# Optimization experiments

Hardware: AMD Instinct MI355X
Metric: run time of the kernel (lower is better)

Reference implementation:

```python
import jax, jax.numpy as jnp
import numpy as np

K = 20
EPS = 1e-5

def get_graph_feature(x, k):
    # x: [B, C, N] -> edge features [B, 2C, N, k]
    xt = jnp.swapaxes(x, 1, 2)  # [B, N, C]
    sq = jnp.sum(xt * xt, axis=-1)  # [B, N]
    # negative squared distance: -(|a|^2 + |b|^2 - 2 a.b)
    pair = 2.0 * jnp.einsum('bnc,bmc->bnm', xt, xt) - sq[:, :, None] - sq[:, None, :]
    idx = jax.lax.top_k(pair, k)[1]  # [B, N, k] nearest neighbors (incl. self)
    neigh = jax.vmap(lambda f, i: f[i])(xt, idx)  # [B, N, k, C]
    ctr = xt[:, :, None, :]  # [B, N, 1, C]
    edge = jnp.concatenate([neigh - ctr, jnp.broadcast_to(ctr, neigh.shape)], axis=-1)  # [B,N,k,2C]
    return jnp.transpose(edge, (0, 3, 1, 2))  # [B, 2C, N, k]

def bn_lrelu(y, g, b, axes):
    # training-mode batchnorm (biased batch stats) + LeakyReLU(0.2)
    m = jnp.mean(y, axis=axes, keepdims=True)
    v = jnp.var(y, axis=axes, keepdims=True)
    shape = [1, -1] + [1] * (y.ndim - 2)
    yn = (y - m) / jnp.sqrt(v + EPS) * g.reshape(shape) + b.reshape(shape)
    return jnp.where(yn >= 0, yn, 0.2 * yn)

def edge_block(x, w, g, b, k):
    e = get_graph_feature(x, k)           # [B, 2C, N, k]
    y = jnp.einsum('bcnk,oc->bonk', e, w)  # 1x1 conv2d, no bias
    y = bn_lrelu(y, g, b, (0, 2, 3))
    return jnp.max(y, axis=-1)            # max over k -> [B, O, N]

def setup_inputs() -> dict:
    key = jax.random.key(0)
    ks = jax.random.split(key, 8)
    B, N = 8, 1024
    num_features = 256
    def w(k_, o, i):
        return jax.random.normal(k_, (o, i), dtype=jnp.float32) * (1.0 / np.sqrt(i))
    d = {
        'x': jax.random.normal(ks[0], (B, N, 3), dtype=jnp.float32),
        'w1': w(ks[1], 64, 6),   'g1': jnp.ones(64),  'b1': jnp.zeros(64),
        'w2': w(ks[2], 64, 128), 'g2': jnp.ones(64),  'b2': jnp.zeros(64),
        'w3': w(ks[3], 128, 128),'g3': jnp.ones(128), 'b3': jnp.zeros(128),
        'w4': w(ks[4], 256, 256),'g4': jnp.ones(256), 'b4': jnp.zeros(256),
        'w5': w(ks[5], 512, 512),'g5': jnp.ones(512), 'b5': jnp.zeros(512),
        'wemb': w(ks[6], num_features, 512),
    }
    return d

def reference(x, w1, g1, b1, w2, g2, b2, w3, g3, b3, w4, g4, b4, w5, g5, b5, wemb):
    xc = jnp.swapaxes(x, 2, 1)  # [B, 3, N]
    x1 = edge_block(xc, w1, g1, b1, K)  # [B, 64, N]
    x2 = edge_block(x1, w2, g2, b2, K)  # [B, 64, N]
    x3 = edge_block(x2, w3, g3, b3, K)  # [B, 128, N]
    x4 = edge_block(x3, w4, g4, b4, K)  # [B, 256, N]
    cat = jnp.concatenate([x1, x2, x3, x4], axis=1)  # [B, 512, N]
    y = jnp.einsum('bcn,oc->bon', cat, w5)            # 1x1 conv1d
    y = bn_lrelu(y, g5, b5, (0, 2))
    feat = jnp.max(y, axis=-1)  # [B, 512]
    return feat @ wemb.T        # [B, num_features]
```

## Files before the change

### kernel.cpp

```cpp
#include <hip/hip_runtime.h>
#include <hip/hip_bf16.h>
#include <math.h>

#define BB 8
#define NN 1024
#define KNNK 20
#define LDC 512

typedef __attribute__((ext_vector_type(8))) short bfrag8;
typedef __attribute__((ext_vector_type(4))) float facc4;
typedef __attribute__((ext_vector_type(2))) float v2f;

struct bh8 { __hip_bfloat16 h[8]; };

__device__ __forceinline__ bh8 cvt8(float4 a, float4 b) {
    bh8 v;
    v.h[0] = __float2bfloat16(a.x); v.h[1] = __float2bfloat16(a.y);
    v.h[2] = __float2bfloat16(a.z); v.h[3] = __float2bfloat16(a.w);
    v.h[4] = __float2bfloat16(b.x); v.h[5] = __float2bfloat16(b.y);
    v.h[6] = __float2bfloat16(b.z); v.h[7] = __float2bfloat16(b.w);
    return v;
}

template<int CTRL, int RMASK>
__device__ __forceinline__ float fmax_dpp(float x) {
    int xi = __float_as_int(x);
    int yi = __builtin_amdgcn_update_dpp(xi, xi, CTRL, RMASK, 0xF, false);
    return fmaxf(x, __int_as_float(yi));
}

__device__ __forceinline__ float wave_max64(float x) {
    x = fmax_dpp<0x121, 0xF>(x);
    x = fmax_dpp<0x122, 0xF>(x);
    x = fmax_dpp<0x124, 0xF>(x);
    x = fmax_dpp<0x128, 0xF>(x);
    x = fmax_dpp<0x142, 0xA>(x);
    x = fmax_dpp<0x143, 0xC>(x);
    return __int_as_float(__builtin_amdgcn_readlane(__float_as_int(x), 63));
}

__device__ __forceinline__ void select20_pf(float (*dist)[1024],
                                            int q0, int w, int lane,
                                            int* __restrict__ idxout) {
    float d[2][16];
    int   sl[2][16];
#pragma unroll
    for (int qi = 0; qi < 2; qi++) {
        int row = w * 2 + qi;
#pragma unroll
        for (int j = 0; j < 16; j++) { d[qi][j] = dist[row][lane + 64 * j]; sl[qi][j] = j; }
    }
    constexpr unsigned char CA[63] = {
        0,2,4,6,8,10,12,14,
        0,1,4,5,8,9,12,13,
        1,5,9,13,
        0,1,2,3,8,9,10,11,
        2,3,10,11,
        1,3,5,9,11,13,
        0,1,2,3,4,5,6,7,
        4,5,6,7,
        2,3,6,7,10,11,
        1,3,5,7,9,11,13};
    constexpr unsigned char CB[63] = {
        1,3,5,7,9,11,13,15,
        2,3,6,7,10,11,14,15,
        2,6,10,14,
        4,5,6,7,12,13,14,15,
        4,5,12,13,
        2,4,6,10,12,14,
        8,9,10,11,12,13,14,15,
        8,9,10,11,
        4,5,8,9,12,13,
        2,4,6,8,10,12,14};
#pragma unroll
    for (int c = 0; c < 63; c++) {
        const int a = CA[c], bq = CB[c];
#pragma unroll
        for (int qi = 0; qi < 2; qi++) {
            bool sw = d[qi][a] < d[qi][bq];
            float dmx = sw ? d[qi][bq] : d[qi][a];
            float dmn = sw ? d[qi][a]  : d[qi][bq];
            d[qi][a] = dmx; d[qi][bq] = dmn;
            int smx = sw ? sl[qi][bq] : sl[qi][a];
            int smn = sw ? sl[qi][a]  : sl[qi][bq];
            sl[qi][a] = smx; sl[qi][bq] = smn;
        }
    }
    unsigned long long slp[2];
#pragma unroll
    for (int qi = 0; qi < 2; qi++) {
        int row = w * 2 + qi;
#pragma unroll
        for (int j = 0; j < 16; j++) dist[row][j * 64 + lane] = d[qi][j];
        unsigned long long p = 0;
#pragma unroll
        for (int j = 0; j < 16; j++) p |= (unsigned long long)sl[qi][j] << (4 * j);
        slp[qi] = p;
    }
    float head[2] = {d[0][0], d[1][0]};
    float pf[2]   = {d[0][1], d[1][1]};
    int   ptr[2]  = {2, 2};
    for (int t = 0; t < KNNK; t++) {
#pragma unroll
        for (int qi = 0; qi < 2; qi++) {
            int row = w * 2 + qi;
            float bv = wave_max64(head[qi]);
            unsigned long long ball = __ballot(head[qi] == bv);
            int wl = (int)__builtin_ctzll(ball);
            bool win = (lane == wl);
            if (win) {
                idxout[(q0 + row) * KNNK + t] = (int)(slp[qi] & 15ull) * 64 + lane;
            }
            head[qi] = win ? pf[qi] : head[qi];
            slp[qi]  = win ? (slp[qi] >> 4) : slp[qi];
            if (win) {
                int p = ptr[qi];
                pf[qi] = (p < 16) ? dist[row][p * 64 + lane] : -INFINITY;
                ptr[qi] = p + 1;
            }
        }
    }
}

__device__ __forceinline__ void zero_r1(float* r1s, float* r1q, int O, int tid) {
    for (int i = tid; i < 32 * O; i += 256) { r1s[i] = 0.f; r1q[i] = 0.f; }
}

__global__ __launch_bounds__(256, 4) void knn3_fused(const float* __restrict__ x,
                                                     const float* __restrict__ w1,
                                                     float* __restrict__ zf,
                                                     int* __restrict__ idxout,
                                                     float* __restrict__ r1s, float* __restrict__ r1q) {
    __shared__ float dist[8][1024];
    int tid = threadIdx.x;
    int q0 = (blockIdx.x & 7) * 1024 + (blockIdx.x >> 3) * 8;
    int b = q0 >> 10;
    if (blockIdx.x == 0) zero_r1(r1s, r1q, 64, tid);
    const float* xb = x + (size_t)b * NN * 3;
    int lane = tid & 63, w = tid >> 6;
    float qx[8], qy[8], qz[8];
#pragma unroll
    for (int q = 0; q < 8; q++) {
        const float* qr = xb + (size_t)((q0 & (NN - 1)) + q) * 3;
        qx[q] = qr[0]; qy[q] = qr[1]; qz[q] = qr[2];
    }
#pragma unroll
    for (int cq = 0; cq < 4; cq++) {
        int cand = w * 256 + cq * 64 + lane;
        const float* cr = xb + (size_t)cand * 3;
        float cx = cr[0], cy = cr[1], cz = cr[2];
        float sqc = 0.f;
        sqc += cx * cx; sqc += cy * cy; sqc += cz * cz;
#pragma unroll
        for (int q = 0; q < 8; q++) {
            float d = qx[q] * cx + qy[q] * cy + qz[q] * cz;
            dist[q][cand] = 2.f * d - sqc;
        }
    }
    for (int i = tid; i < 8 * 128; i += 256) {
        int lq = i >> 7, j = i & 127;
        const float* wr = w1 + (j < 64 ? j * 6 : (j - 64) * 6 + 3);
        const float* xr = x + (size_t)(q0 + lq) * 3;
        zf[(size_t)(q0 + lq) * 128 + j] = wr[0] * xr[0] + wr[1] * xr[1] + wr[2] * xr[2];
    }
    __syncthreads();
    select20_pf(dist, q0, w, lane, idxout);
}

template<int C>
__device__ __forceinline__ void knn_body(const float* __restrict__ xT,
                                         const float* __restrict__ xt, int off,
                                         const float* __restrict__ sqn,
                                         int* __restrict__ idxout,
                                         float (*dist)[1024],
                                         float* qsT_raw, int knnBlk) {
    float (*qsT)[8] = (float (*)[8])qsT_raw;
    int tid = threadIdx.x;
    int q0 = (knnBlk & 7) * 1024 + (knnBlk >> 3) * 8;
    int b = q0 >> 10;
    const float* xb = xt + (size_t)b * NN * LDC + off;
    for (int j = tid; j < 2 * C; j += 256) {
        int c = j % C, ph = j / C;
        int pb = (q0 & (NN - 1)) + ph * 4;
        float4 v;
        v.x = xb[(size_t)(pb + 0) * LDC + c];
        v.y = xb[(size_t)(pb + 1) * LDC + c];
        v.z = xb[(size_t)(pb + 2) * LDC + c];
        v.w = xb[(size_t)(pb + 3) * LDC + c];
        *(float4*)&qsT[c][ph * 4] = v;
    }
    __syncthreads();
    int lane = tid & 63, w = tid >> 6;
    int cand0 = w * 256 + 4 * lane;
    const float* xTb = xT + (size_t)b * C * 1024;
    float4 sq4 = *(const float4*)(sqn + b * NN + cand0);
    v2f acc2[4][4];
#pragma unroll
    for (int j = 0; j < 4; j++)
#pragma unroll
        for (int p = 0; p < 4; p++) acc2[j][p] = (v2f){0.f, 0.f};
    for (int cg = 0; cg < C / 4; cg++) {
        float4 rch[4];
#pragma unroll
        for (int c = 0; c < 4; c++)
            rch[c] = *(const float4*)(xTb + (size_t)(4 * cg + c) * 1024 + cand0);
#pragma unroll
        for (int c = 0; c < 4; c++) {
            float4 qa = *(const float4*)&qsT[4 * cg + c][0];
            float4 qb = *(const float4*)&qsT[4 * cg + c][4];
            v2f qp[4] = {{qa.x, qa.y}, {qa.z, qa.w}, {qb.x, qb.y}, {qb.z, qb.w}};
            float rj[4] = {rch[c].x, rch[c].y, rch[c].z, rch[c].w};
#pragma unroll
            for (int j = 0; j < 4; j++) {
                v2f rr = {rj[j], rj[j]};
                acc2[j][0] += rr * qp[0];
                acc2[j][1] += rr * qp[1];
                acc2[j][2] += rr * qp[2];
                acc2[j][3] += rr * qp[3];
            }
        }
    }
#pragma unroll
    for (int p = 0; p < 4; p++)
#pragma unroll
        for (int half = 0; half < 2; half++) {
            int q = 2 * p + half;
            float4 dv;
            dv.x = 2.f * acc2[0][p][half] - sq4.x;
            dv.y = 2.f * acc2[1][p][half] - sq4.y;
            dv.z = 2.f * acc2[2][p][half] - sq4.z;
            dv.w = 2.f * acc2[3][p][half] - sq4.w;
            *(float4*)&dist[q][cand0] = dv;
        }
    __syncthreads();
    select20_pf(dist, q0, w, lane, idxout);
}

template<int C, int ZO2>
__global__ __launch_bounds__(256, 4) void knnz_fat(const float* __restrict__ xT,
                                                   const float* __restrict__ xt, int off,
                                                   const float* __restrict__ sqn,
                                                   int* __restrict__ idxout,
                                                   const float* __restrict__ w,
                                                   float* __restrict__ zf,
                                                   float* __restrict__ r1s, float* __restrict__ r1q,
                                                   int Onext) {
    __shared__ float dist[8][1024];
    __shared__ __align__(16) float qsT_raw[C * 8];
    int tid = threadIdx.x;
    if ((int)blockIdx.x < BB * NN / 8) {
        knn_body<C>(xT, xt, off, sqn, idxout, dist, qsT_raw, blockIdx.x);
        return;
    }
    constexpr int ZO = ZO2 / 2;
    int zblk = blockIdx.x - BB * NN / 8;
    if (zblk == 0) zero_r1(r1s, r1q, Onext, tid);
    float (*xs)[C] = (float (*)[C])&dist[0][0];
    int p0 = zblk * 16;
    for (int j = tid; j < 16 * (C / 4); j += 256) {
        int p = j / (C / 4), c4 = j % (C / 4);
        *(float4*)&xs[p][4 * c4] = *(const float4*)(xt + (size_t)(p0 + p) * LDC + off + 4 * c4);
    }
    __syncthreads();
    for (int j = tid; j < ZO2; j += 256) {
        const float* wr = w + (j < ZO ? (size_t)j * 2 * C : (size_t)(j - ZO) * 2 * C + C);
        float acc[16];
#pragma unroll
        for (int p = 0; p < 16; p++) acc[p] = 0.f;
        for (int c4 = 0; c4 < C / 4; c4++) {
            float4 wv = *(const float4*)(wr + 4 * c4);
#pragma unroll
            for (int p = 0; p < 16; p++) {
                float4 xv = *(const float4*)&xs[p][4 * c4];
                acc[p] += wv.x * xv.x + wv.y * xv.y + wv.z * xv.z + wv.w * xv.w;
            }
        }
#pragma unroll
        for (int p = 0; p < 16; p++) zf[(size_t)(p0 + p) * ZO2 + j] = acc[p];
    }
}

template<int C>
__global__ __launch_bounds__(256, 4) void knn_fused(const float* __restrict__ xT,
                                                    const float* __restrict__ xt, int off,
                                                    const float* __restrict__ sqn,
                                                    int* __restrict__ idxout,
                                                    float* __restrict__ r1s, float* __restrict__ r1q,
                                                    int Onext) {
    __shared__ float dist[8][1024];
    __shared__ __align__(16) float qsT_raw[C * 8];
    if (blockIdx.x == 0) zero_r1(r1s, r1q, Onext, threadIdx.x);
    knn_body<C>(xT, xt, off, sqn, idxout, dist, qsT_raw, blockIdx.x);
}

__global__ __launch_bounds__(256) void zgemm4_mfma(const float* __restrict__ xtcat,
                                                   const float* __restrict__ w4,
                                                   __hip_bfloat16* __restrict__ zf4) {
    __shared__ __hip_bfloat16 A[128][72];
    __shared__ __hip_bfloat16 W[128][72];
    int mt = blockIdx.x >> 2, nt = blockIdx.x & 3;
    int tid = threadIdx.x;
    int lane = tid & 63, wvx = tid >> 6;
    int mw = wvx >> 1, nw = wvx & 1;
    int m0 = lane & 15, qd = lane >> 4;
    int r = tid & 127, hf = tid >> 7;
    facc4 acc[4][4];
    facc4 zz = {0.f, 0.f, 0.f, 0.f};
#pragma unroll
    for (int mi = 0; mi < 4; mi++)
#pragma unroll
        for (int ni = 0; ni < 4; ni++) acc[mi][ni] = zz;
    int j = nt * 128 + r;
    const float* wsrc = w4 + (j < 256 ? (size_t)j * 256 : (size_t)(j - 256) * 256 + 128);
    const float* asrc = xtcat + (size_t)(mt * 128 + r) * 512 + 128;
    for (int kc = 0; kc < 2; kc++) {
#pragma unroll
        for (int u = 0; u < 4; u++) {
            int c0 = kc * 64 + hf * 32 + 8 * u;
            float4 a0 = *(const float4*)(asrc + c0);
            float4 a1 = *(const float4*)(asrc + c0 + 4);
            *(bh8*)&A[r][hf * 32 + 8 * u] = cvt8(a0, a1);
            float4 w0 = *(const float4*)(wsrc + c0);
            float4 w1 = *(const float4*)(wsrc + c0 + 4);
            *(bh8*)&W[r][hf * 32 + 8 * u] = cvt8(w0, w1);
        }
        __syncthreads();
#pragma unroll
        for (int kk = 0; kk < 2; kk++) {
            bfrag8 af[4], bf[4];
#pragma unroll
            for (int mi = 0; mi < 4; mi++)
                af[mi] = *(const bfrag8*)&A[64 * mw + 16 * mi + m0][32 * kk + 8 * qd];
#pragma unroll
            for (int ni = 0; ni < 4; ni++)
                bf[ni] = *(const bfrag8*)&W[64 * nw + 16 * ni + m0][32 * kk + 8 * qd];
#pragma unroll
            for (int mi = 0; mi < 4; mi++)
#pragma unroll
                for (int ni = 0; ni < 4; ni++)
                    acc[mi][ni] = __builtin_amdgcn_mfma_f32_16x16x32_bf16(af[mi], bf[ni], acc[mi][ni], 0, 0, 0);
        }
        __syncthreads();
    }
#pragma unroll
    for (int mi = 0; mi < 4; mi++)
#pragma unroll
        for (int ni = 0; ni < 4; ni++)
#pragma unroll
            for (int rg = 0; rg < 4; rg++) {
                int row = mt * 128 + mw * 64 + mi * 16 + qd * 4 + rg;
                int col = nt * 128 + nw * 64 + ni * 16 + m0;
                zf4[(size_t)row * 512 + col] = __float2bfloat16(acc[mi][ni][rg]);
            }
}

template<int O2>
__global__ __launch_bounds__(256) void gatherstats_k(const float* __restrict__ zf,
                                                     const int* __restrict__ idx,
                                                     float* __restrict__ ymax, float* __restrict__ ymin,
                                                     float* __restrict__ r1s, float* __restrict__ r1q) {
    constexpr int O = O2 / 2;
    __shared__ float red_s[4][O], red_q[4][O];
    int wv = threadIdx.x >> 6, lane = threadIdx.x & 63;
    int n = (blockIdx.x & 7) * 1024 + (blockIdx.x >> 3) * 4 + wv;
    int b = n >> 10;
    const float* zbatch = zf + (size_t)b * NN * O2;
    int nb[KNNK];
#pragma unroll
    for (int k = 0; k < KNNK; k++) nb[k] = idx[n * KNNK + k];
#pragma unroll
    for (int ch = 0; ch < O / 64; ch++) {
        int o = ch * 64 + lane;
        float g[KNNK];
#pragma unroll
        for (int k = 0; k < KNNK; k++) g[k] = zbatch[(size_t)nb[k] * O2 + o];
        float mx = -INFINITY, mn = INFINITY, s = 0.f, ss = 0.f;
#pragma unroll
        for (int k = 0; k < KNNK; k++) {
            float v = g[k];
            mx = fmaxf(mx, v); mn = fminf(mn, v); s += v; ss += v * v;
        }
        float zn  = zf[(size_t)n * O2 + o];
        float zbn = zf[(size_t)n * O2 + O + o];
        float d = zbn - zn;
        mx += d; mn += d;
        ss = ss + 2.f * d * s + (float)KNNK * d * d;
        s  = s + (float)KNNK * d;
        ymax[(size_t)n * O + o] = mx;
        ymin[(size_t)n * O + o] = mn;
        red_s[wv][o] = s;
        red_q[wv][o] = ss;
    }
    __syncthreads();
    int bucket = blockIdx.x & 31;
    for (int o = threadIdx.x; o < O; o += 256) {
        float s4 = red_s[0][o] + red_s[1][o] + red_s[2][o] + red_s[3][o];
        float q4 = red_q[0][o] + red_q[1][o] + red_q[2][o] + red_q[3][o];
        atomicAdd(&r1s[(size_t)bucket * O + o], s4);
        atomicAdd(&r1q[(size_t)bucket * O + o], q4);
    }
}

__global__ __launch_bounds__(256) void gatherstats4_k(const __hip_bfloat16* __restrict__ zf4,
                                                      const int* __restrict__ idx,
                                                      float* __restrict__ ymax, float* __restrict__ ymin,
                                                      float* __restrict__ r1s, float* __restrict__ r1q) {
    __shared__ float red_s[4][256], red_q[4][256];
    int wv = threadIdx.x >> 6, lane = threadIdx.x & 63;
    int n = (blockIdx.x & 7) * 1024 + (blockIdx.x >> 3) * 4 + wv;
    int b = n >> 10;
    const __hip_bfloat16* zbatch = zf4 + (size_t)b * NN * 512;
    int nb[KNNK];
#pragma unroll
    for (int k = 0; k < KNNK; k++) nb[k] = idx[n * KNNK + k];
#pragma unroll
    for (int ch = 0; ch < 4; ch++) {
        int o = ch * 64 + lane;
        float g[KNNK];
#pragma unroll
        for (int k = 0; k < KNNK; k++) g[k] = __bfloat162float(zbatch[(size_t)nb[k] * 512 + o]);
        float mx = -INFINITY, mn = INFINITY, s = 0.f, ss = 0.f;
#pragma unroll
        for (int k = 0; k < KNNK; k++) {
            float v = g[k];
            mx = fmaxf(mx, v); mn = fminf(mn, v); s += v; ss += v * v;
        }
        float zn  = __bfloat162float(zf4[(size_t)n * 512 + o]);
        float zbn = __bfloat162float(zf4[(size_t)n * 512 + 256 + o]);
        float d = zbn - zn;
        mx += d; mn += d;
        ss = ss + 2.f * d * s + (float)KNNK * d * d;
        s  = s + (float)KNNK * d;
        ymax[(size_t)n * 256 + o] = mx;
        ymin[(size_t)n * 256 + o] = mn;
        red_s[wv][o] = s;
        red_q[wv][o] = ss;
    }
    __syncthreads();
    int bucket = blockIdx.x & 31;
    for (int o = threadIdx.x; o < 256; o += 256) {
        float s4 = red_s[0][o] + red_s[1][o] + red_s[2][o] + red_s[3][o];
        float q4 = red_q[0][o] + red_q[1][o] + red_q[2][o] + red_q[3][o];
        atomicAdd(&r1s[(size_t)bucket * 256 + o], s4);
        atomicAdd(&r1q[(size_t)bucket * 256 + o], q4);
    }
}

template<int O>
__global__ __launch_bounds__(256) void epitrans2_k(const float* __restrict__ ymax, const float* __restrict__ ymin,
                                                   const float* __restrict__ r1s, const float* __restrict__ r1q,
                                                   const float* __restrict__ g, const float* __restrict__ beta,
                                                   double invM,
                                                   float* __restrict__ xtcat, int off_out,
                                                   float* __restrict__ xT, float* __restrict__ sqn,
                                                   __hip_bfloat16* __restrict__ xbf) {
    __shared__ float tile[64][O + 1];
    __shared__ float ssh[O], tth[O];
    int n0 = blockIdx.x * 64;
    int b = n0 >> 10;
    int tid = threadIdx.x;
    for (int o = tid; o < O; o += 256) {
        double sd = 0.0, qd = 0.0;
        for (int r = 0; r < 32; r++) { sd += r1s[(size_t)r * O + o]; qd += r1q[(size_t)r * O + o]; }
        double mean = sd * invM;
        double var = qd * invM - mean * mean;
        float inv = (float)(1.0 / sqrt(var + 1e-5));
        float sc = g[o] * inv;
        ssh[o] = sc;
        tth[o] = beta[o] - (float)mean * sc;
    }
    __syncthreads();
    for (int i = tid; i < 64 * O; i += 256) {
        int nl = i / O;
        int o = i & (O - 1);
        int n = n0 + nl;
        float sc = ssh[o];
        float v = sc >= 0.f ? ymax[(size_t)n * O + o] : ymin[(size_t)n * O + o];
        float y = sc * v + tth[o];
        y = y >= 0.f ? y : 0.2f * y;
        xtcat[(size_t)n * LDC + off_out + o] = y;
        xbf[(size_t)n * LDC + off_out + o] = __float2bfloat16(y);
        tile[nl][o] = y;
    }
    __syncthreads();
    if (tid < 64) {
        float sq = 0.f;
        for (int c = 0; c < O; c++) { float v = tile[tid][c]; sq += v * v; }
        sqn[n0 + tid] = sq;
    }
    int r = tid >> 4, cq = tid & 15;
#pragma unroll
    for (int ct = 0; ct < O / 16; ct++) {
        int c = ct * 16 + r;
        float4 ov;
        ov.x = tile[4 * cq + 0][c];
        ov.y = tile[4 * cq + 1][c];
        ov.z = tile[4 * cq + 2][c];
        ov.w = tile[4 * cq + 3][c];
        *(float4*)(xT + ((size_t)b * O + c) * 1024 + (n0 & (NN - 1)) + 4 * cq) = ov;
    }
}

__global__ __launch_bounds__(256) void epilogue4_k(const float* __restrict__ ymax, const float* __restrict__ ymin,
                                                   const float* __restrict__ r1s, const float* __restrict__ r1q,
                                                   const float* __restrict__ g, const float* __restrict__ beta,
                                                   double invM,
                                                   __hip_bfloat16* __restrict__ xbf) {
    __shared__ float ssh[256], tth[256];
    int n0 = blockIdx.x * 64;
    int tid = threadIdx.x;
    {
        int o = tid;
        double sd = 0.0, qd = 0.0;
        for (int r = 0; r < 32; r++) { sd += r1s[(size_t)r * 256 + o]; qd += r1q[(size_t)r * 256 + o]; }
        double mean = sd * invM;
        double var = qd * invM - mean * mean;
        float inv = (float)(1.0 / sqrt(var + 1e-5));
        float sc = g[o] * inv;
        ssh[o] = sc;
        tth[o] = beta[o] - (float)mean * sc;
    }
    __syncthreads();
    for (int i = tid; i < 64 * 256; i += 256) {
        int nl = i >> 8;
        int o = i & 255;
        int n = n0 + nl;
        float sc = ssh[o];
        float v = sc >= 0.f ? ymax[(size_t)n * 256 + o] : ymin[(size_t)n * 256 + o];
        float y = sc * v + tth[o];
        y = y >= 0.f ? y : 0.2f * y;
        xbf[(size_t)n * LDC + 256 + o] = __float2bfloat16(y);
    }
}

__global__ __launch_bounds__(256) void gemm5_mfma(const __hip_bfloat16* __restrict__ xbf,
                                                  const float* __restrict__ w5,
                                                  float* __restrict__ pmax, float* __restrict__ pmn,
                                                  float* __restrict__ ps, float* __restrict__ pq) {
    __shared__ __hip_bfloat16 A[128][72];
    __shared__ __hip_bfloat16 W[128][72];
    int mt = blockIdx.x >> 2, nt = blockIdx.x & 3;
    int tid = threadIdx.x;
    int lane = tid & 63, wvx = tid >> 6;
    int mw = wvx >> 1, nw = wvx & 1;
    int m0 = lane & 15, qd = lane >> 4;
    int r = tid & 127, hf = tid >> 7;
    facc4 acc[4][4];
    facc4 zz = {0.f, 0.f, 0.f, 0.f};
#pragma unroll
    for (int mi = 0; mi < 4; mi++)
#pragma unroll
        for (int ni = 0; ni < 4; ni++) acc[mi][ni] = zz;
    for (int kc = 0; kc < 8; kc++) {
        const __hip_bfloat16* ap = xbf + (size_t)(mt * 128 + r) * 512 + kc * 64 + hf * 32;
        const float* wp = w5 + (size_t)(nt * 128 + r) * 512 + kc * 64 + hf * 32;
#pragma unroll
        for (int u = 0; u < 4; u++) {
            bh8 av = *(const bh8*)(ap + 8 * u);
            *(bh8*)&A[r][hf * 32 + 8 * u] = av;
            float4 w0 = *(const float4*)(wp + 8 * u);
            float4 w1 = *(const float4*)(wp + 8 * u + 4);
            *(bh8*)&W[r][hf * 32 + 8 * u] = cvt8(w0, w1);
        }
        __syncthreads();
#pragma unroll
        for (int kk = 0; kk < 2; kk++) {
            bfrag8 af[4], bf[4];
#pragma unroll
            for (int mi = 0; mi < 4; mi++)
                af[mi] = *(const bfrag8*)&A[64 * mw + 16 * mi + m0][32 * kk + 8 * qd];
#pragma unroll
            for (int ni = 0; ni < 4; ni++)
                bf[ni] = *(const bfrag8*)&W[64 * nw + 16 * ni + m0][32 * kk + 8 * qd];
#pragma unroll
            for (int mi = 0; mi < 4; mi++)
#pragma unroll
                for (int ni = 0; ni < 4; ni++)
                    acc[mi][ni] = __builtin_amdgcn_mfma_f32_16x16x32_bf16(af[mi], bf[ni], acc[mi][ni], 0, 0, 0);
        }
        __syncthreads();
    }
#pragma unroll
    for (int mi = 0; mi < 4; mi++) {
        int grp = mt * 8 + mw * 4 + mi;
#pragma unroll
        for (int ni = 0; ni < 4; ni++) {
            float mx = -INFINITY, mn = INFINITY, s = 0.f, ss = 0.f;
#pragma unroll
            for (int rg = 0; rg < 4; rg++) {
                float v = acc[mi][ni][rg];
                mx = fmaxf(mx, v); mn = fminf(mn, v); s += v; ss += v * v;
            }
#pragma unroll
            for (int m = 16; m < 64; m <<= 1) {
                mx = fmaxf(mx, __shfl_xor(mx, m));
                mn = fminf(mn, __shfl_xor(mn, m));
                s += __shfl_xor(s, m);
                ss += __shfl_xor(ss, m);
            }
            if (qd == 0) {
                int o = nt * 128 + nw * 64 + ni * 16 + m0;
                pmax[(size_t)grp * 512 + o] = mx;
                pmn [(size_t)grp * 512 + o] = mn;
                ps  [(size_t)grp * 512 + o] = s;
                pq  [(size_t)grp * 512 + o] = ss;
            }
        }
    }
}

__global__ __launch_bounds__(256) void bnstat5_k(const float* __restrict__ ps, const float* __restrict__ pq,
                                                 const float* __restrict__ g, const float* __restrict__ beta,
                                                 float* __restrict__ s_out, float* __restrict__ t_out) {
    __shared__ double lds_s[4][8], lds_q[4][8];
    int tid = threadIdx.x;
    int lane = tid & 63, wv = tid >> 6;
    int ol = lane & 7;
    int rg = wv * 8 + (lane >> 3);
    int o = blockIdx.x * 8 + ol;
    double s = 0.0, q = 0.0;
    for (int r = rg; r < 512; r += 32) {
        s += ps[(size_t)r * 512 + o];
        q += pq[(size_t)r * 512 + o];
    }
    s += __shfl_xor(s, 8);  q += __shfl_xor(q, 8);
    s += __shfl_xor(s, 16); q += __shfl_xor(q, 16);
    s += __shfl_xor(s, 32); q += __shfl_xor(q, 32);
    if (lane < 8) { lds_s[wv][ol] = s; lds_q[wv][ol] = q; }
    __syncthreads();
    if (tid < 8) {
        s = lds_s[0][tid] + lds_s[1][tid] + lds_s[2][tid] + lds_s[3][tid];
        q = lds_q[0][tid] + lds_q[1][tid] + lds_q[2][tid] + lds_q[3][tid];
        double invM = 1.0 / (BB * NN);
        double mean = s * invM;
        double var = q * invM - mean * mean;
        float inv = (float)(1.0 / sqrt(var + 1e-5));
        int oo = blockIdx.x * 8 + tid;
        float sc = g[oo] * inv;
        s_out[oo] = sc;
        t_out[oo] = beta[oo] - (float)mean * sc;
    }
}

__global__ __launch_bounds__(256) void featreduce_k(const float* __restrict__ pmax, const float* __restrict__ pmn,
                                                    const float* __restrict__ s, const float* __restrict__ t,
                                                    float* __restrict__ feat8) {
    __shared__ float smx[4][64], smn[4][64];
    int blk = blockIdx.x;
    int b = blk >> 3, oc = blk & 7;
    int tid = threadIdx.x;
    int lane = tid & 63, wv = tid >> 6;
    int o = oc * 64 + lane;
    float mx = -INFINITY, mn = INFINITY;
    for (int r = b * 64 + wv; r < (b + 1) * 64; r += 4) {
        mx = fmaxf(mx, pmax[(size_t)r * 512 + o]);
        mn = fminf(mn, pmn [(size_t)r * 512 + o]);
    }
    smx[wv][lane] = mx; smn[wv][lane] = mn;
    __syncthreads();
    if (wv == 0) {
        mx = fmaxf(fmaxf(smx[0][lane], smx[1][lane]), fmaxf(smx[2][lane], smx[3][lane]));
        mn = fminf(fminf(smn[0][lane], smn[1][lane]), fminf(smn[2][lane], smn[3][lane]));
        float sc = s[o];
        float v = sc >= 0.f ? mx : mn;
        float y = sc * v + t[o];
        feat8[(size_t)b * 512 + o] = y >= 0.f ? y : 0.2f * y;
    }
}

__global__ __launch_bounds__(256) void outgemm_k(const float* __restrict__ feat8,
                                                 const float* __restrict__ wemb,
                                                 float* __restrict__ out) {
    __shared__ __align__(16) float feat[512];
    int blk = blockIdx.x;
    int b = blk >> 3, nc = blk & 7;
    int tid = threadIdx.x;
    for (int i = tid; i < 512; i += 256) feat[i] = feat8[(size_t)b * 512 + i];
    __syncthreads();
    int o_l = tid >> 3, kc = tid & 7;
    int o = nc * 32 + o_l;
    const float4* wr = (const float4*)(wemb + (size_t)o * 512 + kc * 64);
    const float4* fv = (const float4*)(feat + kc * 64);
    float acc = 0.f;
#pragma unroll
    for (int i = 0; i < 16; i++) {
        float4 wv = wr[i];
        float4 f  = fv[i];
        acc += wv.x * f.x + wv.y * f.y + wv.z * f.z + wv.w * f.w;
    }
    acc += __shfl_xor(acc, 1);
    acc += __shfl_xor(acc, 2);
    acc += __shfl_xor(acc, 4);
    if (kc == 0) out[(size_t)b * 256 + o] = acc;
}

extern "C" void kernel_launch(void* const* d_in, const int* in_sizes, int n_in,
                              void* d_out, int out_size, void* d_ws, size_t ws_size,
                              hipStream_t stream) {
    const float* x    = (const float*)d_in[0];
    const float* w1   = (const float*)d_in[1];
    const float* g1   = (const float*)d_in[2];
    const float* b1   = (const float*)d_in[3];
    const float* w2   = (const float*)d_in[4];
    const float* g2   = (const float*)d_in[5];
    const float* b2   = (const float*)d_in[6];
    const float* w3   = (const float*)d_in[7];
    const float* g3   = (const float*)d_in[8];
    const float* b3   = (const float*)d_in[9];
    const float* w4   = (const float*)d_in[10];
    const float* g4   = (const float*)d_in[11];
    const float* b4   = (const float*)d_in[12];
    const float* w5   = (const float*)d_in[13];
    const float* g5   = (const float*)d_in[14];
    const float* b5   = (const float*)d_in[15];
    const float* wemb = (const float*)d_in[16];
    float* out = (float*)d_out;

    float* fws    = (float*)d_ws;
    float* xtcat  = fws;
    float* ymax   = xtcat + (size_t)BB * NN * 512;
    float* ymin   = ymax + (size_t)BB * NN * 256;
    float* psum   = ymin + (size_t)BB * NN * 256;
    float* psumsq = psum + (size_t)BB * NN * 256;
    float* xT     = psum;
    float* pmax   = ymax;
    float* pmn    = pmax + 512 * 512;
    float* ps5    = pmn + 512 * 512;
    float* pq5    = ps5 + 512 * 512;
    float* feat8  = psumsq;
    float* sqn    = psumsq + (size_t)BB * NN * 256;
    float* s_arr  = sqn + BB * NN;
    float* t_arr  = s_arr + 512;
    float* r1s    = t_arr + 512;
    float* r1q    = r1s + 32 * 512;
    int*   idxb   = (int*)(r1q + 32 * 512);
    float* zfull  = (float*)(idxb + BB * NN * KNNK);
    __hip_bfloat16* zf4 = (__hip_bfloat16*)zfull;
    __hip_bfloat16* xbf = (__hip_bfloat16*)(zfull + (size_t)BB * NN * 512);

    const double invM_edge = 1.0 / ((double)BB * NN * KNNK);
    const int nbn = BB * NN;
    const int NK = nbn / 8;
    const int NZ = nbn / 16;

    knn3_fused<<<NK, 256, 0, stream>>>(x, w1, zfull, idxb, r1s, r1q);
    gatherstats_k<128><<<nbn / 4, 256, 0, stream>>>(zfull, idxb, ymax, ymin, r1s, r1q);
    epitrans2_k<64><<<128, 256, 0, stream>>>(ymax, ymin, r1s, r1q, g1, b1, invM_edge, xtcat, 0, xT, sqn, xbf);

    knnz_fat<64, 128><<<NK + NZ, 256, 0, stream>>>(xT, xtcat, 0, sqn, idxb, w2, zfull, r1s, r1q, 64);
    gatherstats_k<128><<<nbn / 4, 256, 0, stream>>>(zfull, idxb, ymax, ymin, r1s, r1q);
    epitrans2_k<64><<<128, 256, 0, stream>>>(ymax, ymin, r1s, r1q, g2, b2, invM_edge, xtcat, 64, xT, sqn, xbf);

    knnz_fat<64, 256><<<NK + NZ, 256, 0, stream>>>(xT, xtcat, 64, sqn, idxb, w3, zfull, r1s, r1q, 128);
    gatherstats_k<256><<<nbn / 4, 256, 0, stream>>>(zfull, idxb, ymax, ymin, r1s, r1q);
    epitrans2_k<128><<<128, 256, 0, stream>>>(ymax, ymin, r1s, r1q, g3, b3, invM_edge, xtcat, 128, xT, sqn, xbf);

    knn_fused<128><<<NK, 256, 0, stream>>>(xT, xtcat, 128, sqn, idxb, r1s, r1q, 256);
    zgemm4_mfma<<<256, 256, 0, stream>>>(xtcat, w4, zf4);
    gatherstats4_k<<<nbn / 4, 256, 0, stream>>>(zf4, idxb, ymax, ymin, r1s, r1q);
    epilogue4_k<<<128, 256, 0, stream>>>(ymax, ymin, r1s, r1q, g4, b4, invM_edge, xbf);

    gemm5_mfma<<<256, 256, 0, stream>>>(xbf, w5, pmax, pmn, ps5, pq5);
    bnstat5_k<<<64, 256, 0, stream>>>(ps5, pq5, g5, b5, s_arr, t_arr);
    featreduce_k<<<64, 256, 0, stream>>>(pmax, pmn, s_arr, t_arr, feat8);
    outgemm_k<<<64, 256, 0, stream>>>(feat8, wemb, out);
}
```

Before: 344.7 us.

## Fuse layer-4 kNN with z-GEMM and read query points straight from global

Merges the layer-4 kNN kernel and the MFMA z-GEMM into one launch, with extra blocks doing the GEMM and the LDS shared between the two roles through one byte buffer. This removes a launch and lets the two independent jobs run side by side. In kNN, the query features are no longer staged into LDS with a transposed load and barrier. They are read as float4 directly from the transposed xT array in global memory, which saves the LDS footprint and a sync but relies on cache hits for those reads.

```diff
diff --git a/kernel.cpp b/kernel.cpp
--- a/kernel.cpp
+++ b/kernel.cpp
@@ -169,30 +169,16 @@
 
 template<int C>
 __device__ __forceinline__ void knn_body(const float* __restrict__ xT,
-                                         const float* __restrict__ xt, int off,
                                          const float* __restrict__ sqn,
                                          int* __restrict__ idxout,
-                                         float (*dist)[1024],
-                                         float* qsT_raw, int knnBlk) {
-    float (*qsT)[8] = (float (*)[8])qsT_raw;
+                                         float (*dist)[1024], int knnBlk) {
     int tid = threadIdx.x;
     int q0 = (knnBlk & 7) * 1024 + (knnBlk >> 3) * 8;
     int b = q0 >> 10;
-    const float* xb = xt + (size_t)b * NN * LDC + off;
-    for (int j = tid; j < 2 * C; j += 256) {
-        int c = j % C, ph = j / C;
-        int pb = (q0 & (NN - 1)) + ph * 4;
-        float4 v;
-        v.x = xb[(size_t)(pb + 0) * LDC + c];
-        v.y = xb[(size_t)(pb + 1) * LDC + c];
-        v.z = xb[(size_t)(pb + 2) * LDC + c];
-        v.w = xb[(size_t)(pb + 3) * LDC + c];
-        *(float4*)&qsT[c][ph * 4] = v;
-    }
-    __syncthreads();
     int lane = tid & 63, w = tid >> 6;
     int cand0 = w * 256 + 4 * lane;
     const float* xTb = xT + (size_t)b * C * 1024;
+    const float* qrow = xTb + (q0 & (NN - 1));
     float4 sq4 = *(const float4*)(sqn + b * NN + cand0);
     v2f acc2[4][4];
 #pragma unroll
@@ -206,8 +192,9 @@
             rch[c] = *(const float4*)(xTb + (size_t)(4 * cg + c) * 1024 + cand0);
 #pragma unroll
         for (int c = 0; c < 4; c++) {
-            float4 qa = *(const float4*)&qsT[4 * cg + c][0];
-            float4 qb = *(const float4*)&qsT[4 * cg + c][4];
+            const float* qr = qrow + (size_t)(4 * cg + c) * 1024;
+            float4 qa = *(const float4*)qr;
+            float4 qb = *(const float4*)(qr + 4);
             v2f qp[4] = {{qa.x, qa.y}, {qa.z, qa.w}, {qb.x, qb.y}, {qb.z, qb.w}};
             float rj[4] = {rch[c].x, rch[c].y, rch[c].z, rch[c].w};
 #pragma unroll
@@ -246,10 +233,9 @@
                                                    float* __restrict__ r1s, float* __restrict__ r1q,
                                                    int Onext) {
     __shared__ float dist[8][1024];
-    __shared__ __align__(16) float qsT_raw[C * 8];
     int tid = threadIdx.x;
     if ((int)blockIdx.x < BB * NN / 8) {
-        knn_body<C>(xT, xt, off, sqn, idxout, dist, qsT_raw, blockIdx.x);
+        knn_body<C>(xT, sqn, idxout, dist, blockIdx.x);
         return;
     }
     constexpr int ZO = ZO2 / 2;
@@ -280,26 +266,25 @@
     }
 }
 
-template<int C>
-__global__ __launch_bounds__(256, 4) void knn_fused(const float* __restrict__ xT,
-                                                    const float* __restrict__ xt, int off,
+__global__ __launch_bounds__(256, 4) void knnz4_fat(const float* __restrict__ xT,
                                                     const float* __restrict__ sqn,
                                                     int* __restrict__ idxout,
-                                                    float* __restrict__ r1s, float* __restrict__ r1q,
-                                                    int Onext) {
-    __shared__ float dist[8][1024];
-    __shared__ __align__(16) float qsT_raw[C * 8];
-    if (blockIdx.x == 0) zero_r1(r1s, r1q, Onext, threadIdx.x);
-    knn_body<C>(xT, xt, off, sqn, idxout, dist, qsT_raw, blockIdx.x);
-}
-
-__global__ __launch_bounds__(256) void zgemm4_mfma(const float* __restrict__ xtcat,
-                                                   const float* __restrict__ w4,
-                                                   __hip_bfloat16* __restrict__ zf4) {
-    __shared__ __hip_bfloat16 A[128][72];
-    __shared__ __hip_bfloat16 W[128][72];
-    int mt = blockIdx.x >> 2, nt = blockIdx.x & 3;
-    int tid = threadIdx.x;
+                                                    const float* __restrict__ xtcat,
+                                                    const float* __restrict__ w4,
+                                                    __hip_bfloat16* __restrict__ zf4,
+                                                    float* __restrict__ r1s, float* __restrict__ r1q) {
+    __shared__ __align__(16) char smem[36864];
+    int tid = threadIdx.x;
+    if ((int)blockIdx.x < BB * NN / 8) {
+        float (*dist)[1024] = (float (*)[1024])smem;
+        if (blockIdx.x == 0) zero_r1(r1s, r1q, 256, tid);
+        knn_body<128>(xT, sqn, idxout, dist, blockIdx.x);
+        return;
+    }
+    __hip_bfloat16 (*A)[72] = (__hip_bfloat16 (*)[72])smem;
+    __hip_bfloat16 (*W)[72] = (__hip_bfloat16 (*)[72])(smem + 18432);
+    int zblk = blockIdx.x - BB * NN / 8;
+    int mt = zblk >> 2, nt = zblk & 3;
     int lane = tid & 63, wvx = tid >> 6;
     int mw = wvx >> 1, nw = wvx & 1;
     int m0 = lane & 15, qd = lane >> 4;
@@ -755,8 +740,7 @@
     gatherstats_k<256><<<nbn / 4, 256, 0, stream>>>(zfull, idxb, ymax, ymin, r1s, r1q);
     epitrans2_k<128><<<128, 256, 0, stream>>>(ymax, ymin, r1s, r1q, g3, b3, invM_edge, xtcat, 128, xT, sqn, xbf);
 
-    knn_fused<128><<<NK, 256, 0, stream>>>(xT, xtcat, 128, sqn, idxb, r1s, r1q, 256);
-    zgemm4_mfma<<<256, 256, 0, stream>>>(xtcat, w4, zf4);
+    knnz4_fat<<<NK + 256, 256, 0, stream>>>(xT, sqn, idxb, xtcat, w4, zf4, r1s, r1q);
     gatherstats4_k<<<nbn / 4, 256, 0, stream>>>(zf4, idxb, ymax, ymin, r1s, r1q);
     epilogue4_k<<<128, 256, 0, stream>>>(ymax, ymin, r1s, r1q, g4, b4, invM_edge, xbf);
 
```

New measurement: 330.7 us. -4.1%, faster.
